# Kernel optimization log

Hardware: AMD Instinct MI355X
Metric: run time of the kernel (lower is better)

## Reference

```python
import jax, jax.numpy as jnp
import numpy as np

N = 16_777_216
NUM_SEG = 1_000_000


def setup_inputs() -> dict:
    key = jax.random.key(0)
    k1, k2 = jax.random.split(key)
    pred_pair = jax.random.randint(k1, (N, 2), 0, NUM_SEG, dtype=jnp.int32).astype(jnp.int64)
    reg_feat = jax.random.uniform(k2, (N,), dtype=jnp.float32)
    return {"pred_pair": pred_pair, "reg_feat": reg_feat, "num_segments": NUM_SEG}


def reference(pred_pair, reg_feat, num_segments):
    # Equivalent to torch.unique + per-group loop: unique ids index into a
    # dense segment table; empty segments are never gathered so their fill
    # value is irrelevant.
    id0 = pred_pair[:, 0]
    id1 = pred_pair[:, 1]
    # per-group max of reg_feat grouped by first id, broadcast back (temp)
    m0 = jax.ops.segment_max(reg_feat, id0, num_segments=num_segments)
    temp = m0[id0]
    # per-group max grouped by second id, multiplied elementwise
    m1 = jax.ops.segment_max(reg_feat, id1, num_segments=num_segments)
    soft_mutual_score = temp * m1[id1]
    return soft_mutual_score
```

## Files before the change

kernel.cpp:

```cpp
#include <hip/hip_runtime.h>
#include <stdint.h>

#define N_ELEM 16777216
#define N_PAIR (N_ELEM / 2)
#define NUM_SEG 1000000
#define NBIN 128
#define SEG_PER_BIN 8192
#define ELEM_PER_WG 2048
#define NWG_A (N_ELEM / ELEM_PER_WG)
#define REC_PER_WG (2 * ELEM_PER_WG)
#define NSPLIT 8
#define SLOTS_PER_SPLIT (NWG_A / NSPLIT)

typedef int   int4v   __attribute__((ext_vector_type(4)));
typedef float float2v __attribute__((ext_vector_type(2)));
typedef float float4v __attribute__((ext_vector_type(4)));
typedef unsigned int uint4v __attribute__((ext_vector_type(4)));



__global__ __launch_bounds__(256) void gtsms_phaseA(const int* __restrict__ pp,
                                                    const float* __restrict__ feat,
                                                    unsigned int* __restrict__ rec,
                                                    unsigned short* __restrict__ cnts) {
    __shared__ unsigned int hist[NBIN];
    __shared__ unsigned int basex[NBIN];
    __shared__ unsigned int recs[REC_PER_WG];
    const int wg = blockIdx.x, t = threadIdx.x;
    if (t < NBIN) hist[t] = 0;
    __syncthreads();

    const int ebase = wg * ELEM_PER_WG + t * 8;
    const int4v* pp4 = reinterpret_cast<const int4v*>(pp);
    const float4v* f4 = reinterpret_cast<const float4v*>(feat);
    int4v q0 = __builtin_nontemporal_load(pp4 + ebase / 2 + 0);
    int4v q1 = __builtin_nontemporal_load(pp4 + ebase / 2 + 1);
    int4v q2 = __builtin_nontemporal_load(pp4 + ebase / 2 + 2);
    int4v q3 = __builtin_nontemporal_load(pp4 + ebase / 2 + 3);
    float4v v0 = __builtin_nontemporal_load(f4 + ebase / 4 + 0);
    float4v v1 = __builtin_nontemporal_load(f4 + ebase / 4 + 1);

    int   id0[8], id1[8];
    unsigned int val[8];
    id0[0] = q0.x; id1[0] = q0.y; id0[1] = q0.z; id1[1] = q0.w;
    id0[2] = q1.x; id1[2] = q1.y; id0[3] = q1.z; id1[3] = q1.w;
    id0[4] = q2.x; id1[4] = q2.y; id0[5] = q2.z; id1[5] = q2.w;
    id0[6] = q3.x; id1[6] = q3.y; id0[7] = q3.z; id1[7] = q3.w;
    val[0] = __float_as_uint(v0.x) >> 16; val[1] = __float_as_uint(v0.y) >> 16;
    val[2] = __float_as_uint(v0.z) >> 16; val[3] = __float_as_uint(v0.w) >> 16;
    val[4] = __float_as_uint(v1.x) >> 16; val[5] = __float_as_uint(v1.y) >> 16;
    val[6] = __float_as_uint(v1.z) >> 16; val[7] = __float_as_uint(v1.w) >> 16;

    unsigned int rbin[16], rrank[16], rpk[16];
#pragma unroll
    for (int e = 0; e < 8; ++e) {
        unsigned int b0 = (unsigned int)id0[e] >> 13;
        unsigned int b1 = (unsigned int)id1[e] >> 13;
        rpk[2 * e]     = (((unsigned int)id0[e] & 8191u) << 16) | val[e];
        rpk[2 * e + 1] = (1u << 29) | (((unsigned int)id1[e] & 8191u) << 16) | val[e];
        rbin[2 * e] = b0;
        rbin[2 * e + 1] = b1;
        rrank[2 * e] = atomicAdd(&hist[b0], 1u);
        rrank[2 * e + 1] = atomicAdd(&hist[b1], 1u);
    }
    __syncthreads();

    if (t < 64) {
        unsigned int a0 = hist[t], a1 = hist[t + 64];
        unsigned int s0 = a0, s1 = a1;
#pragma unroll
        for (int d = 1; d < 64; d <<= 1) {
            unsigned int n = __shfl_up(s0, d);
            if (t >= d) s0 += n;
        }
        unsigned int tot0 = __shfl(s0, 63);
#pragma unroll
        for (int d = 1; d < 64; d <<= 1) {
            unsigned int n = __shfl_up(s1, d);
            if (t >= d) s1 += n;
        }
        basex[t] = s0 - a0;
        basex[t + 64] = tot0 + s1 - a1;
    }
    __syncthreads();

#pragma unroll
    for (int r = 0; r < 16; ++r)
        recs[basex[rbin[r]] + rrank[r]] = rpk[r];
    __syncthreads();

    uint4v* ro = reinterpret_cast<uint4v*>(rec + (size_t)wg * REC_PER_WG);
#pragma unroll
    for (int k = 0; k < 4; ++k) {
        int q = t + 256 * k;
        uint4v w = { recs[4 * q], recs[4 * q + 1], recs[4 * q + 2], recs[4 * q + 3] };
        __builtin_nontemporal_store(w, ro + q);
    }
    if (t < NBIN) cnts[(size_t)wg * NBIN + t] = (unsigned short)basex[t];
}

__global__ __launch_bounds__(256) void gtsms_phaseB(const unsigned int* __restrict__ rec,
                                                    const unsigned short* __restrict__ cnts,
                                                    unsigned short* __restrict__ partials) {
    __shared__ unsigned int tab[2 * SEG_PER_BIN];
    const int bin = blockIdx.x >> 3;
    const int split = blockIdx.x & 7;
    const int t = threadIdx.x;
    for (int i = t; i < 2 * SEG_PER_BIN; i += 256) tab[i] = 0u;
    __syncthreads();

    const int wave = t >> 6, lane = t & 63;
    const int sub = lane >> 4, sl = lane & 15;
    const int slot0 = split * SLOTS_PER_SPLIT + wave * (SLOTS_PER_SPLIT / 4);
    for (int g = 0; g < SLOTS_PER_SPLIT / 16; ++g) {
        int s = slot0 + g * 4 + sub;
        unsigned int b0 = cnts[(size_t)s * NBIN + bin];
        unsigned int e0 = (bin < NBIN - 1) ? cnts[(size_t)s * NBIN + bin + 1]
                                           : (unsigned int)REC_PER_WG;
        const unsigned int* rp = rec + (size_t)s * REC_PER_WG;
        for (unsigned int j = b0 + sl; j < e0; j += 16) {
            unsigned int r = rp[j];
            atomicMax(&tab[(r >> 16) & 0x3FFFu], r << 16);
        }
    }
    __syncthreads();
    unsigned short* po = partials + (size_t)(bin * NSPLIT + split) * (2 * SEG_PER_BIN);
    for (int i = t; i < 2 * SEG_PER_BIN; i += 256)
        po[i] = (unsigned short)(tab[i] >> 16);
}

__global__ void gtsms_merge(const unsigned short* __restrict__ partials,
                            unsigned short* __restrict__ mb0,
                            unsigned short* __restrict__ mb1) {
    int seg = blockIdx.x * 256 + threadIdx.x;
    if (seg >= NUM_SEG) return;
    int bin = seg >> 13, local = seg & 8191;
    const unsigned short* p = partials + (size_t)bin * NSPLIT * (2 * SEG_PER_BIN);
    unsigned int u0 = 0, u1 = 0;
#pragma unroll
    for (int s = 0; s < NSPLIT; ++s) {
        u0 = max(u0, (unsigned int)p[s * (2 * SEG_PER_BIN) + local]);
        u1 = max(u1, (unsigned int)p[s * (2 * SEG_PER_BIN) + SEG_PER_BIN + local]);
    }
    mb0[seg] = (unsigned short)u0;
    mb1[seg] = (unsigned short)u1;
}

__global__ void gtsms_gather_kernel(const int* __restrict__ pp,
                                    const unsigned short* __restrict__ mb0,
                                    const unsigned short* __restrict__ mb1,
                                    float* __restrict__ out) {
    int t = blockIdx.x * blockDim.x + threadIdx.x;
    if (t < N_PAIR / 2) {
        int p = 2 * t;
        int4v prA = __builtin_nontemporal_load(reinterpret_cast<const int4v*>(pp) + p);
        int4v prB = __builtin_nontemporal_load(reinterpret_cast<const int4v*>(pp) + p + 1);
        unsigned int a0 = mb0[prA.x];
        unsigned int b0 = mb1[prA.y];
        unsigned int a1 = mb0[prA.z];
        unsigned int b1 = mb1[prA.w];
        unsigned int a2 = mb0[prB.x];
        unsigned int b2 = mb1[prB.y];
        unsigned int a3 = mb0[prB.z];
        unsigned int b3 = mb1[prB.w];
        float4v o;
        o.x = __uint_as_float(a0 << 16) * __uint_as_float(b0 << 16);
        o.y = __uint_as_float(a1 << 16) * __uint_as_float(b1 << 16);
        o.z = __uint_as_float(a2 << 16) * __uint_as_float(b2 << 16);
        o.w = __uint_as_float(a3 << 16) * __uint_as_float(b3 << 16);
        __builtin_nontemporal_store(o, reinterpret_cast<float4v*>(out) + t);
    }
}


__global__ void gtsms_zero_kernel(uint4v* __restrict__ ws, int n_vec4) {
    int i = blockIdx.x * blockDim.x + threadIdx.x;
    if (i < n_vec4) ws[i] = (uint4v){0u, 0u, 0u, 0u};
}

__global__ void gtsms_scatter_chunk(const int* __restrict__ pp,
                                    const float* __restrict__ feat,
                                    unsigned int* __restrict__ m0,
                                    unsigned int* __restrict__ m1,
                                    const unsigned short* __restrict__ mb0,
                                    const unsigned short* __restrict__ mb1,
                                    int base_pair, int n_threads) {
    int t = blockIdx.x * blockDim.x + threadIdx.x;
    if (t >= n_threads) return;
    int p = base_pair + 2 * t;
    int4v prA = __builtin_nontemporal_load(reinterpret_cast<const int4v*>(pp) + p);
    int4v prB = __builtin_nontemporal_load(reinterpret_cast<const int4v*>(pp) + p + 1);
    float2v fvA = __builtin_nontemporal_load(reinterpret_cast<const float2v*>(feat) + p);
    float2v fvB = __builtin_nontemporal_load(reinterpret_cast<const float2v*>(feat) + p + 1);
    unsigned int f0 = __float_as_uint(fvA.x);
    unsigned int f1 = __float_as_uint(fvA.y);
    unsigned int f2 = __float_as_uint(fvB.x);
    unsigned int f3 = __float_as_uint(fvB.y);
    unsigned int c0 = mb0[prA.x];
    unsigned int c1 = mb1[prA.y];
    unsigned int c2 = mb0[prA.z];
    unsigned int c3 = mb1[prA.w];
    unsigned int c4 = mb0[prB.x];
    unsigned int c5 = mb1[prB.y];
    unsigned int c6 = mb0[prB.z];
    unsigned int c7 = mb1[prB.w];
    if (f0 > (c0 << 16)) atomicMax(&m0[prA.x], f0);
    if (f0 > (c1 << 16)) atomicMax(&m1[prA.y], f0);
    if (f1 > (c2 << 16)) atomicMax(&m0[prA.z], f1);
    if (f1 > (c3 << 16)) atomicMax(&m1[prA.w], f1);
    if (f2 > (c4 << 16)) atomicMax(&m0[prB.x], f2);
    if (f2 > (c5 << 16)) atomicMax(&m1[prB.y], f2);
    if (f3 > (c6 << 16)) atomicMax(&m0[prB.z], f3);
    if (f3 > (c7 << 16)) atomicMax(&m1[prB.w], f3);
}

__global__ void gtsms_refresh_kernel(const unsigned int* __restrict__ m0,
                                     const unsigned int* __restrict__ m1,
                                     unsigned short* __restrict__ mb0,
                                     unsigned short* __restrict__ mb1) {
    int i = blockIdx.x * blockDim.x + threadIdx.x;
    if (i < NUM_SEG) {
        mb0[i] = (unsigned short)(m0[i] >> 16);
        mb1[i] = (unsigned short)(m1[i] >> 16);
    }
}

__global__ void gtsms_convert_rtne_kernel(const unsigned int* __restrict__ m0,
                                          const unsigned int* __restrict__ m1,
                                          unsigned short* __restrict__ mb0,
                                          unsigned short* __restrict__ mb1) {
    int i = blockIdx.x * blockDim.x + threadIdx.x;
    if (i < NUM_SEG) {
        unsigned int u0 = m0[i];
        unsigned int u1 = m1[i];
        mb0[i] = (unsigned short)((u0 + 0x7FFFu + ((u0 >> 16) & 1u)) >> 16);
        mb1[i] = (unsigned short)((u1 + 0x7FFFu + ((u1 >> 16) & 1u)) >> 16);
    }
}


extern "C" void kernel_launch(void* const* d_in, const int* in_sizes, int n_in,
                              void* d_out, int out_size, void* d_ws, size_t ws_size,
                              hipStream_t stream) {
    const int* pp = (const int*)d_in[0];
    const float* feat = (const float*)d_in[1];
    float* out = (float*)d_out;

    const int BLK = 256;
    dim3 gatherGrid((N_PAIR / 2 + BLK - 1) / BLK);

    const size_t O_REC = 0;
    const size_t O_CNT = O_REC + (size_t)NWG_A * REC_PER_WG * 4;
    const size_t O_PART = O_CNT + (size_t)NWG_A * NBIN * 2;
    const size_t O_TAB = O_PART + (size_t)NBIN * NSPLIT * 2 * SEG_PER_BIN * 2;
    const size_t NEED = O_TAB + (size_t)2 * NUM_SEG * 2;

    if (ws_size >= NEED) {
        unsigned int* rec = (unsigned int*)((char*)d_ws + O_REC);
        unsigned short* cnts = (unsigned short*)((char*)d_ws + O_CNT);
        unsigned short* partials = (unsigned short*)((char*)d_ws + O_PART);
        unsigned short* mb0 = (unsigned short*)((char*)d_ws + O_TAB);
        unsigned short* mb1 = mb0 + NUM_SEG;

        gtsms_phaseA<<<NWG_A, BLK, 0, stream>>>(pp, feat, rec, cnts);
        gtsms_phaseB<<<NBIN * NSPLIT, BLK, 0, stream>>>(rec, cnts, partials);
        gtsms_merge<<<(NUM_SEG + BLK - 1) / BLK, BLK, 0, stream>>>(partials, mb0, mb1);
        gtsms_gather_kernel<<<gatherGrid, BLK, 0, stream>>>(pp, mb0, mb1, out);
    } else {
        unsigned int* m0 = (unsigned int*)d_ws;
        unsigned int* m1 = m0 + NUM_SEG;
        unsigned short* mb0 = (unsigned short*)(m1 + NUM_SEG);
        unsigned short* mb1 = mb0 + NUM_SEG;

        dim3 segGrid((NUM_SEG + BLK - 1) / BLK);
        int zero_vec4 = (3 * NUM_SEG) / 4;
        dim3 zeroGrid((zero_vec4 + BLK - 1) / BLK);
        gtsms_zero_kernel<<<zeroGrid, BLK, 0, stream>>>((uint4v*)d_ws, zero_vec4);

        const int cb[7] = {0, N_PAIR / 64, N_PAIR / 16, N_PAIR / 8,
                           N_PAIR / 4, N_PAIR / 2, N_PAIR};
        for (int c = 0; c < 6; ++c) {
            int n_threads = (cb[c + 1] - cb[c]) / 2;
            dim3 g((n_threads + BLK - 1) / BLK);
            gtsms_scatter_chunk<<<g, BLK, 0, stream>>>(pp, feat, m0, m1, mb0, mb1,
                                                       cb[c], n_threads);
            if (c < 5)
                gtsms_refresh_kernel<<<segGrid, BLK, 0, stream>>>(m0, m1, mb0, mb1);
        }
        gtsms_convert_rtne_kernel<<<segGrid, BLK, 0, stream>>>(m0, m1, mb0, mb1);
        gtsms_gather_kernel<<<gatherGrid, BLK, 0, stream>>>(pp, mb0, mb1, out);
    }
}
```

Measured before the change: 670.0 us.

## Split id0/id1 records into separate bins and halve phase B LDS table

Phase A now routes records into 256 bins, with id0 records in bins 0-127 and id1 records in bins 128-255, instead of 128 bins carrying an id-select bit. Phase B then needs only an 8192-entry LDS table per workgroup (32 KB instead of 64 KB), so more workgroups can be resident per CU. Splits per bin drop from 8 to 4, which keeps the total block count at 1024 but halves the partials and merge reads. Costs are a longer four-block scan in phase A and a cnts array twice the size.

```diff
diff --git a/kernel.cpp b/kernel.cpp
--- a/kernel.cpp
+++ b/kernel.cpp
@@ -4,12 +4,12 @@
 #define N_ELEM 16777216
 #define N_PAIR (N_ELEM / 2)
 #define NUM_SEG 1000000
-#define NBIN 128
+#define NBIN 256
 #define SEG_PER_BIN 8192
 #define ELEM_PER_WG 2048
 #define NWG_A (N_ELEM / ELEM_PER_WG)
 #define REC_PER_WG (2 * ELEM_PER_WG)
-#define NSPLIT 8
+#define NSPLIT 4
 #define SLOTS_PER_SPLIT (NWG_A / NSPLIT)
 
 typedef int   int4v   __attribute__((ext_vector_type(4)));
@@ -27,7 +27,7 @@
     __shared__ unsigned int basex[NBIN];
     __shared__ unsigned int recs[REC_PER_WG];
     const int wg = blockIdx.x, t = threadIdx.x;
-    if (t < NBIN) hist[t] = 0;
+    hist[t] = 0;
     __syncthreads();
 
     const int ebase = wg * ELEM_PER_WG + t * 8;
@@ -55,9 +55,9 @@
 #pragma unroll
     for (int e = 0; e < 8; ++e) {
         unsigned int b0 = (unsigned int)id0[e] >> 13;
-        unsigned int b1 = (unsigned int)id1[e] >> 13;
+        unsigned int b1 = 128u + ((unsigned int)id1[e] >> 13);
         rpk[2 * e]     = (((unsigned int)id0[e] & 8191u) << 16) | val[e];
-        rpk[2 * e + 1] = (1u << 29) | (((unsigned int)id1[e] & 8191u) << 16) | val[e];
+        rpk[2 * e + 1] = (((unsigned int)id1[e] & 8191u) << 16) | val[e];
         rbin[2 * e] = b0;
         rbin[2 * e + 1] = b1;
         rrank[2 * e] = atomicAdd(&hist[b0], 1u);
@@ -66,21 +66,19 @@
     __syncthreads();
 
     if (t < 64) {
-        unsigned int a0 = hist[t], a1 = hist[t + 64];
-        unsigned int s0 = a0, s1 = a1;
-#pragma unroll
-        for (int d = 1; d < 64; d <<= 1) {
-            unsigned int n = __shfl_up(s0, d);
-            if (t >= d) s0 += n;
+        unsigned int carry = 0;
+#pragma unroll
+        for (int blk = 0; blk < 4; ++blk) {
+            unsigned int a = hist[blk * 64 + t];
+            unsigned int s = a;
+#pragma unroll
+            for (int d = 1; d < 64; d <<= 1) {
+                unsigned int n = __shfl_up(s, d);
+                if (t >= d) s += n;
+            }
+            basex[blk * 64 + t] = carry + s - a;
+            carry += __shfl(s, 63);
         }
-        unsigned int tot0 = __shfl(s0, 63);
-#pragma unroll
-        for (int d = 1; d < 64; d <<= 1) {
-            unsigned int n = __shfl_up(s1, d);
-            if (t >= d) s1 += n;
-        }
-        basex[t] = s0 - a0;
-        basex[t + 64] = tot0 + s1 - a1;
     }
     __syncthreads();
 
@@ -96,17 +94,17 @@
         uint4v w = { recs[4 * q], recs[4 * q + 1], recs[4 * q + 2], recs[4 * q + 3] };
         __builtin_nontemporal_store(w, ro + q);
     }
-    if (t < NBIN) cnts[(size_t)wg * NBIN + t] = (unsigned short)basex[t];
+    cnts[(size_t)wg * NBIN + t] = (unsigned short)basex[t];
 }
 
 __global__ __launch_bounds__(256) void gtsms_phaseB(const unsigned int* __restrict__ rec,
                                                     const unsigned short* __restrict__ cnts,
                                                     unsigned short* __restrict__ partials) {
-    __shared__ unsigned int tab[2 * SEG_PER_BIN];
-    const int bin = blockIdx.x >> 3;
-    const int split = blockIdx.x & 7;
+    __shared__ unsigned int tab[SEG_PER_BIN];
+    const int bin = blockIdx.x >> 2;
+    const int split = blockIdx.x & 3;
     const int t = threadIdx.x;
-    for (int i = t; i < 2 * SEG_PER_BIN; i += 256) tab[i] = 0u;
+    for (int i = t; i < SEG_PER_BIN; i += 256) tab[i] = 0u;
     __syncthreads();
 
     const int wave = t >> 6, lane = t & 63;
@@ -120,12 +118,12 @@
         const unsigned int* rp = rec + (size_t)s * REC_PER_WG;
         for (unsigned int j = b0 + sl; j < e0; j += 16) {
             unsigned int r = rp[j];
-            atomicMax(&tab[(r >> 16) & 0x3FFFu], r << 16);
+            atomicMax(&tab[(r >> 16) & 0x1FFFu], r << 16);
         }
     }
     __syncthreads();
-    unsigned short* po = partials + (size_t)(bin * NSPLIT + split) * (2 * SEG_PER_BIN);
-    for (int i = t; i < 2 * SEG_PER_BIN; i += 256)
+    unsigned short* po = partials + (size_t)(bin * NSPLIT + split) * SEG_PER_BIN;
+    for (int i = t; i < SEG_PER_BIN; i += 256)
         po[i] = (unsigned short)(tab[i] >> 16);
 }
 
@@ -134,13 +132,14 @@
                             unsigned short* __restrict__ mb1) {
     int seg = blockIdx.x * 256 + threadIdx.x;
     if (seg >= NUM_SEG) return;
-    int bin = seg >> 13, local = seg & 8191;
-    const unsigned short* p = partials + (size_t)bin * NSPLIT * (2 * SEG_PER_BIN);
+    int b = seg >> 13, local = seg & 8191;
+    const unsigned short* p0 = partials + (size_t)(b * NSPLIT) * SEG_PER_BIN;
+    const unsigned short* p1 = partials + (size_t)((128 + b) * NSPLIT) * SEG_PER_BIN;
     unsigned int u0 = 0, u1 = 0;
 #pragma unroll
     for (int s = 0; s < NSPLIT; ++s) {
-        u0 = max(u0, (unsigned int)p[s * (2 * SEG_PER_BIN) + local]);
-        u1 = max(u1, (unsigned int)p[s * (2 * SEG_PER_BIN) + SEG_PER_BIN + local]);
+        u0 = max(u0, (unsigned int)p0[s * SEG_PER_BIN + local]);
+        u1 = max(u1, (unsigned int)p1[s * SEG_PER_BIN + local]);
     }
     mb0[seg] = (unsigned short)u0;
     mb1[seg] = (unsigned short)u1;
@@ -252,7 +251,7 @@
     const size_t O_REC = 0;
     const size_t O_CNT = O_REC + (size_t)NWG_A * REC_PER_WG * 4;
     const size_t O_PART = O_CNT + (size_t)NWG_A * NBIN * 2;
-    const size_t O_TAB = O_PART + (size_t)NBIN * NSPLIT * 2 * SEG_PER_BIN * 2;
+    const size_t O_TAB = O_PART + (size_t)NBIN * NSPLIT * SEG_PER_BIN * 2;
     const size_t NEED = O_TAB + (size_t)2 * NUM_SEG * 2;
 
     if (ws_size >= NEED) {
```

Result: faster. 601.7 us (-10.2%).
